# Kernel tuning notes

Hardware: AMD Instinct MI355X
Metric: run time of the kernel (lower is better)

The kernel has to match this reference:

```python
import jax, jax.numpy as jnp
import numpy as np

USER_NUM = 100000
ITEM_NUM = 50000
N_EDGES = 2000000
EMB = 64
N_LAYERS = 3


def setup_inputs() -> dict:
    key = jax.random.key(0)
    k1, k2, k3, k4 = jax.random.split(key, 4)
    # xavier-uniform-like init scale for embeddings
    scale = float(np.sqrt(6.0 / (USER_NUM + EMB)))
    user_emb = jax.random.uniform(k1, (USER_NUM, EMB), jnp.float32, -scale, scale)
    scale_i = float(np.sqrt(6.0 / (ITEM_NUM + EMB)))
    item_emb = jax.random.uniform(k2, (ITEM_NUM, EMB), jnp.float32, -scale_i, scale_i)
    u_idx = jax.random.randint(k3, (N_EDGES,), 0, USER_NUM, jnp.int32)
    i_idx = jax.random.randint(k4, (N_EDGES,), 0, ITEM_NUM, jnp.int32)
    return {"user_emb": user_emb, "item_emb": item_emb, "u_idx": u_idx, "i_idx": i_idx}


def _degree_norms(u_idx, i_idx):
    ones = jnp.ones(u_idx.shape[0], jnp.float32)
    d_u = jax.ops.segment_sum(ones, u_idx, num_segments=USER_NUM)
    d_i = jax.ops.segment_sum(ones, i_idx, num_segments=ITEM_NUM)
    d_u = jnp.where(d_u == 0, 1.0, d_u)
    d_i = jnp.where(d_i == 0, 1.0, d_i)
    return ((1.0 / d_u)[:, None], (1.0 / d_i)[:, None],
            (d_u ** -0.5)[:, None], (d_i ** -0.5)[:, None])


def reference(user_emb, item_emb, u_idx, i_idx):
    d_u_inv, d_i_inv, d_u_inv_sqrt, d_i_inv_sqrt = _degree_norms(u_idx, i_idx)

    # SpMM via gather + segment_sum on the edge list (binary interaction values)
    def spmm_rt(x_u):  # (rt @ x_u): [U,D] -> [I,D]
        return jax.ops.segment_sum(x_u[u_idx], i_idx, num_segments=ITEM_NUM)

    def spmm_r(x_i):  # (r @ x_i): [I,D] -> [U,D]
        return jax.ops.segment_sum(x_i[i_idx], u_idx, num_segments=USER_NUM)

    user_e = user_emb
    item_e = item_emb
    sum_u = user_e
    sum_i = item_e
    for _ in range(N_LAYERS):
        # user propagation: u -> hyperedge(items) -> u
        tmp_u = user_e * d_u_inv_sqrt
        tmp_i = spmm_rt(tmp_u) * d_i_inv
        user_e = spmm_r(tmp_i) * d_u_inv_sqrt
        sum_u = sum_u + user_e
        # item propagation: i -> hyperedge(users) -> i
        tmp_i2 = item_e * d_i_inv_sqrt
        tmp_u2 = spmm_r(tmp_i2) * d_u_inv
        item_e = spmm_rt(tmp_u2) * d_i_inv_sqrt
        sum_i = sum_i + item_e
    inv = 1.0 / (N_LAYERS + 1)
    return sum_u * inv, sum_i * inv
```

## Files before the change

kernel.cpp:

```cpp
#include <hip/hip_runtime.h>
#include <hip/hip_fp16.h>
#include <math.h>

#define U_NUM 100000
#define I_NUM 50000
#define NE    2000000
#define EMB   64
#define NLAYERS 3

#define BSH   9
#define BROWS 512
#define NBU_U ((U_NUM + 511) >> 9)
#define NBU_I ((I_NUM + 511) >> 9)
#define NBU_T (NBU_U + NBU_I)
#define CHUNK 8192
#define NBLK_E ((NE + CHUNK - 1) / CHUNK)
#define DBINS 512
#define PACK_SH 17
#define PACK_MASK 0x1FFFF

#define FP8_SCALE 512.0f

typedef float v2f __attribute__((ext_vector_type(2)));

static inline int ceil_div(int a, int b){ return (a + b - 1) / b; }


__global__ void hist_k(const int* __restrict__ u_idx, const int* __restrict__ i_idx,
                       int* __restrict__ cm_u, int* __restrict__ cm_i,
                       int* __restrict__ dhist_u, int* __restrict__ dhist_i){
  if (blockIdx.x == 0){
    for (int t = threadIdx.x; t < DBINS; t += 256) dhist_u[t] = 0;
  } else if (blockIdx.x == 1){
    for (int t = threadIdx.x; t < DBINS; t += 256) dhist_i[t] = 0;
  }
  __shared__ int h[NBU_T];
  for (int t = threadIdx.x; t < NBU_T; t += 256) h[t] = 0;
  __syncthreads();
  int base = blockIdx.x * CHUNK;
  int end = min(base + CHUNK, NE);
  for (int e = base + (threadIdx.x << 1); e < end; e += 512){
    int2 uu = *(const int2*)(u_idx + e);
    int2 ii = *(const int2*)(i_idx + e);
    atomicAdd(&h[uu.x >> BSH], 1);
    atomicAdd(&h[uu.y >> BSH], 1);
    atomicAdd(&h[NBU_U + (ii.x >> BSH)], 1);
    atomicAdd(&h[NBU_U + (ii.y >> BSH)], 1);
  }
  __syncthreads();
  for (int t = threadIdx.x; t < NBU_U; t += 256) cm_u[blockIdx.x * NBU_U + t] = h[t];
  for (int t = threadIdx.x; t < NBU_I; t += 256) cm_i[blockIdx.x * NBU_I + t] = h[NBU_U + t];
}

__global__ void colsum_k(const int* __restrict__ cm_u, const int* __restrict__ cm_i,
                         int* __restrict__ tot_u, int* __restrict__ tot_i){
  __shared__ int s[256];
  int j = blockIdx.x;
  const int* cm; int* tot; int jj, stride;
  if (j < NBU_U){ cm = cm_u; tot = tot_u; jj = j; stride = NBU_U; }
  else { cm = cm_i; tot = tot_i; jj = j - NBU_U; stride = NBU_I; }
  int acc = 0;
  for (int b = threadIdx.x; b < NBLK_E; b += 256) acc += cm[b * stride + jj];
  s[threadIdx.x] = acc; __syncthreads();
  for (int o = 128; o > 0; o >>= 1){
    if (threadIdx.x < o) s[threadIdx.x] += s[threadIdx.x + o];
    __syncthreads();
  }
  if (threadIdx.x == 0) tot[jj] = s[0];
}

__global__ void small_scan2_k(const int* __restrict__ cA, int* __restrict__ oA,
                              int* __restrict__ rA, int nA,
                              const int* __restrict__ cB, int* __restrict__ oB,
                              int* __restrict__ rB, int nB){
  const int* cnt; int* offs; int* cur; int n;
  if (blockIdx.x == 0){ cnt = cA; offs = oA; cur = rA; n = nA; }
  else { cnt = cB; offs = oB; cur = rB; n = nB; }
  __shared__ int s[1024];
  int t = threadIdx.x;
  int v = (t < n) ? cnt[t] : 0;
  s[t] = v; __syncthreads();
  for (int o = 1; o < 1024; o <<= 1){
    int x = (t >= o) ? s[t - o] : 0;
    __syncthreads();
    s[t] += x;
    __syncthreads();
  }
  int excl = (t > 0) ? s[t - 1] : 0;
  if (t < n){ offs[t] = excl; cur[t] = excl; }
  if (t == n - 1) offs[n] = s[t];
}

__global__ void colscan_k(const int* __restrict__ cm_u, const int* __restrict__ cm_i,
                          const int* __restrict__ boffs_u, const int* __restrict__ boffs_i,
                          int* __restrict__ bm_u, int* __restrict__ bm_i){
  __shared__ int s[256];
  int j = blockIdx.x;
  const int* cm; const int* boffs; int* bm; int jj, stride;
  if (j < NBU_U){ cm = cm_u; boffs = boffs_u; bm = bm_u; jj = j; stride = NBU_U; }
  else { cm = cm_i; boffs = boffs_i; bm = bm_i; jj = j - NBU_U; stride = NBU_I; }
  int t = threadIdx.x;
  int v = (t < NBLK_E) ? cm[t * stride + jj] : 0;
  s[t] = v; __syncthreads();
  for (int o = 1; o < 256; o <<= 1){
    int x = (t >= o) ? s[t - o] : 0;
    __syncthreads();
    s[t] += x;
    __syncthreads();
  }
  int excl = (t > 0) ? s[t - 1] : 0;
  if (t < NBLK_E) bm[t * stride + jj] = excl + boffs[jj];
}


__global__ void binfill_k(const int* __restrict__ u_idx, const int* __restrict__ i_idx,
                          const int* __restrict__ bm_u, const int* __restrict__ bm_i,
                          int* __restrict__ bin_u, int* __restrict__ bin_i){
  __shared__ int cur[NBU_T];
  for (int t = threadIdx.x; t < NBU_U; t += 256) cur[t] = bm_u[blockIdx.x * NBU_U + t];
  for (int t = threadIdx.x; t < NBU_I; t += 256) cur[NBU_U + t] = bm_i[blockIdx.x * NBU_I + t];
  __syncthreads();
  int base = blockIdx.x * CHUNK;
  int end = min(base + CHUNK, NE);
  for (int e = base + (threadIdx.x << 1); e < end; e += 512){
    int2 uu = *(const int2*)(u_idx + e);
    int2 ii = *(const int2*)(i_idx + e);
    int p;
    p = atomicAdd(&cur[uu.x >> BSH], 1);            bin_u[p] = ((uu.x & 511) << PACK_SH) | ii.x;
    p = atomicAdd(&cur[uu.y >> BSH], 1);            bin_u[p] = ((uu.y & 511) << PACK_SH) | ii.y;
    p = atomicAdd(&cur[NBU_U + (ii.x >> BSH)], 1);  bin_i[p] = ((ii.x & 511) << PACK_SH) | uu.x;
    p = atomicAdd(&cur[NBU_U + (ii.y >> BSH)], 1);  bin_i[p] = ((ii.y & 511) << PACK_SH) | uu.y;
  }
}


__global__ void bucket_build_k(const int* __restrict__ bin_u, const int* __restrict__ bin_i,
                               const int* __restrict__ boffs_u, const int* __restrict__ boffs_i,
                               int* __restrict__ cnt_u, int* __restrict__ cnt_i,
                               int* __restrict__ offs_u, int* __restrict__ offs_i,
                               float* __restrict__ du_inv, float* __restrict__ du_invs,
                               float* __restrict__ di_inv, float* __restrict__ di_invs,
                               int* __restrict__ adj_u, int* __restrict__ adj_i,
                               int* __restrict__ dhist_u, int* __restrict__ dhist_i){
  __shared__ int h[BROWS];
  __shared__ int part[256];
  __shared__ int dh[DBINS];
  int b = blockIdx.x;
  const int* bin; const int* boffs; int* cnt; int* offs; float* inv; float* invs;
  int* adj; int* dhist; int jj, nrows;
  if (b < NBU_U){
    bin = bin_u; boffs = boffs_u; cnt = cnt_u; offs = offs_u;
    inv = du_inv; invs = du_invs; adj = adj_u; dhist = dhist_u; jj = b; nrows = U_NUM;
  } else {
    bin = bin_i; boffs = boffs_i; cnt = cnt_i; offs = offs_i;
    inv = di_inv; invs = di_invs; adj = adj_i; dhist = dhist_i; jj = b - NBU_U; nrows = I_NUM;
  }
  int tid = threadIdx.x;
  int r0 = jj << BSH;
  int beg = boffs[jj], end = boffs[jj + 1];
  h[2*tid] = 0; h[2*tid + 1] = 0;
  for (int t = tid; t < DBINS; t += 256) dh[t] = 0;
  __syncthreads();
  for (int e = beg + tid; e < end; e += 256)
    atomicAdd(&h[((unsigned)bin[e]) >> PACK_SH], 1);
  __syncthreads();
  int c0 = h[2*tid], c1 = h[2*tid + 1];
  part[tid] = c0 + c1; __syncthreads();
  for (int o = 1; o < 256; o <<= 1){
    int x = (tid >= o) ? part[tid - o] : 0;
    __syncthreads();
    part[tid] += x;
    __syncthreads();
  }
  int excl = (tid > 0) ? part[tid - 1] : 0;
  h[2*tid] = excl;
  h[2*tid + 1] = excl + c0;
#pragma unroll
  for (int k = 0; k < 2; ++k){
    int l = 2*tid + k;
    int row = r0 + l;
    int c = k ? c1 : c0;
    int o = k ? (excl + c0) : excl;
    if (row < nrows){
      cnt[row] = c;
      offs[row] = beg + o;
      float d = (c > 0) ? (float)c : 1.0f;
      inv[row]  = 1.0f / d;
      invs[row] = 1.0f / sqrtf(d);
      atomicAdd(&dh[min(c, DBINS - 1)], 1);
    } else if (row == nrows){
      offs[row] = beg + o;
    }
  }
  __syncthreads();
  for (int e = beg + tid; e < end; e += 256){
    int v = bin[e];
    int slot = beg + atomicAdd(&h[((unsigned)v) >> PACK_SH], 1);
    adj[slot] = v & PACK_MASK;
  }
  __syncthreads();
  for (int t = tid; t < DBINS; t += 256) if (dh[t]) atomicAdd(&dhist[t], dh[t]);
}


__global__ void deg_scatter_k(const int* __restrict__ cnt, const int* __restrict__ offs,
                              int* __restrict__ dcur, int4* __restrict__ rd, int n){
  __shared__ int h[DBINS];
  __shared__ int base_s[DBINS];
  for (int t = threadIdx.x; t < DBINS; t += 256) h[t] = 0;
  __syncthreads();
  int base = blockIdx.x * 2048;
  int end = min(base + 2048, n);
  for (int r = base + threadIdx.x; r < end; r += 256)
    atomicAdd(&h[min(cnt[r], DBINS - 1)], 1);
  __syncthreads();
  for (int t = threadIdx.x; t < DBINS; t += 256){
    int c = h[t];
    base_s[t] = c ? atomicAdd(&dcur[t], c) : 0;
    h[t] = 0;
  }
  __syncthreads();
  for (int r = base + threadIdx.x; r < end; r += 256){
    int c = cnt[r];
    int b = min(c, DBINS - 1);
    int pos = base_s[b] + atomicAdd(&h[b], 1);
    int bg = offs[r];
    rd[n - 1 - pos] = make_int4(bg, bg + c, r, 0);
  }
}


__device__ __forceinline__ unsigned pack4_fp8(float a, float b, float c, float d){
  int p = 0;
  p = __builtin_amdgcn_cvt_pk_fp8_f32(a, b, p, false);
  p = __builtin_amdgcn_cvt_pk_fp8_f32(c, d, p, true);
  return (unsigned)p;
}

__device__ __forceinline__ void accq(float* a, uint2 q){
  v2f f0 = __builtin_amdgcn_cvt_pk_f32_fp8(q.x, false);
  v2f f1 = __builtin_amdgcn_cvt_pk_f32_fp8(q.x, true);
  v2f f2 = __builtin_amdgcn_cvt_pk_f32_fp8(q.y, false);
  v2f f3 = __builtin_amdgcn_cvt_pk_f32_fp8(q.y, true);
  a[0] += f0.x; a[1] += f0.y; a[2] += f1.x; a[3] += f1.y;
  a[4] += f2.x; a[5] += f2.y; a[6] += f3.x; a[7] += f3.y;
}


__global__ void init_k(const float* __restrict__ ue, const float* __restrict__ ie,
                       const float* __restrict__ dus, const float* __restrict__ dis,
                       float* __restrict__ out, unsigned char* __restrict__ ue8,
                       unsigned char* __restrict__ ie8){
  int idx4 = blockIdx.x * blockDim.x + threadIdx.x;
  const int nu4 = U_NUM * (EMB / 4);
  const int tot4 = (U_NUM + I_NUM) * (EMB / 4);
  if (idx4 >= tot4) return;
  const float* e; unsigned char* hp; float s; int loc;
  if (idx4 < nu4){ e = ue; hp = ue8; loc = idx4; s = dus[idx4 >> 4] * FP8_SCALE; }
  else { e = ie; hp = ie8; loc = idx4 - nu4; s = dis[(idx4 - nu4) >> 4] * FP8_SCALE; }
  float4 v = ((const float4*)e)[loc];
  float4 o = make_float4(v.x * 0.25f, v.y * 0.25f, v.z * 0.25f, v.w * 0.25f);
  ((float4*)out)[idx4] = o;
  ((unsigned*)hp)[loc] = pack4_fp8(v.x * s, v.y * s, v.z * s, v.w * s);
}


template<bool HAS_SUM>
__global__ void spmm_pair(
    const int4* __restrict__ rdA, const int* __restrict__ adjA,
    const unsigned char* __restrict__ srcA, const float* __restrict__ psA, const float* __restrict__ phA,
    unsigned char* __restrict__ dstA, float* __restrict__ sumA, int nA,
    const int4* __restrict__ rdB, const int* __restrict__ adjB,
    const unsigned char* __restrict__ srcB, const float* __restrict__ psB, const float* __restrict__ phB,
    unsigned char* __restrict__ dstB, float* __restrict__ sumB, int nB){
  int t = blockIdx.x * blockDim.x + threadIdx.x;
  int rid = t >> 3;
  int lane = t & 7;
  const int4* rd; const int* adj; const unsigned char* src; const float* ps; const float* ph;
  unsigned char* dst; float* sum;
  if (rid < nA){
    rd = rdA; adj = adjA; src = srcA; ps = psA; ph = phA; dst = dstA; sum = sumA;
  } else {
    rid -= nA;
    if (rid >= nB) return;
    rd = rdB; adj = adjB; src = srcB; ps = psB; ph = phB; dst = dstB; sum = sumB;
  }
  int4 d = rd[rid];
  int beg = d.x, end = d.y, row = d.z;
  const unsigned char* sp8 = src + (size_t)(lane << 3);
  float acc[8];
#pragma unroll
  for (int k = 0; k < 8; ++k) acc[k] = 0.f;
  int j = beg;
  for (; j + 7 < end; j += 8){
    int n0 = adj[j],   n1 = adj[j+1], n2 = adj[j+2], n3 = adj[j+3];
    int n4 = adj[j+4], n5 = adj[j+5], n6 = adj[j+6], n7 = adj[j+7];
    uint2 q0 = *(const uint2*)(sp8 + (((size_t)n0) << 6));
    uint2 q1 = *(const uint2*)(sp8 + (((size_t)n1) << 6));
    uint2 q2 = *(const uint2*)(sp8 + (((size_t)n2) << 6));
    uint2 q3 = *(const uint2*)(sp8 + (((size_t)n3) << 6));
    uint2 q4 = *(const uint2*)(sp8 + (((size_t)n4) << 6));
    uint2 q5 = *(const uint2*)(sp8 + (((size_t)n5) << 6));
    uint2 q6 = *(const uint2*)(sp8 + (((size_t)n6) << 6));
    uint2 q7 = *(const uint2*)(sp8 + (((size_t)n7) << 6));
    accq(acc, q0); accq(acc, q1); accq(acc, q2); accq(acc, q3);
    accq(acc, q4); accq(acc, q5); accq(acc, q6); accq(acc, q7);
  }
  for (; j < end; ++j){
    int n0 = adj[j];
    uint2 q0 = *(const uint2*)(sp8 + (((size_t)n0) << 6));
    accq(acc, q0);
  }
  float phv = ph[row];
  unsigned lo = pack4_fp8(acc[0] * phv, acc[1] * phv, acc[2] * phv, acc[3] * phv);
  unsigned hi = pack4_fp8(acc[4] * phv, acc[5] * phv, acc[6] * phv, acc[7] * phv);
  *(uint2*)(dst + (((size_t)row) << 6) + (size_t)(lane << 3)) = make_uint2(lo, hi);
  if (HAS_SUM){
    float psv = ps[row] * (0.25f / FP8_SCALE);
    float4* sp = (float4*)(sum + (((size_t)row) << 6) + (size_t)(lane << 3));
#pragma unroll
    for (int k = 0; k < 2; ++k){
      float4 s = sp[k];
      s.x += acc[4*k]     * psv;
      s.y += acc[4*k + 1] * psv;
      s.z += acc[4*k + 2] * psv;
      s.w += acc[4*k + 3] * psv;
      sp[k] = s;
    }
  }
}


extern "C" void kernel_launch(void* const* d_in, const int* in_sizes, int n_in,
                              void* d_out, int out_size, void* d_ws, size_t ws_size,
                              hipStream_t stream){
  const float* user_emb = (const float*)d_in[0];
  const float* item_emb = (const float*)d_in[1];
  const int*   u_idx    = (const int*)d_in[2];
  const int*   i_idx    = (const int*)d_in[3];
  float* out = (float*)d_out;

  char* w = (char*)d_ws;
  size_t off = 0;
  auto alloc = [&](size_t bytes) -> void* {
    void* p = (void*)(w + off);
    off += (bytes + 255) & ~(size_t)255;
    return p;
  };
  int* cnt_u   = (int*)alloc((size_t)U_NUM * 4);
  int* cnt_i   = (int*)alloc((size_t)I_NUM * 4);
  int* offs_u  = (int*)alloc((size_t)(U_NUM + 1) * 4);
  int* offs_i  = (int*)alloc((size_t)(I_NUM + 1) * 4);
  int* cm_u    = (int*)alloc((size_t)NBLK_E * NBU_U * 4);
  int* cm_i    = (int*)alloc((size_t)NBLK_E * NBU_I * 4);
  int* bm_u    = (int*)alloc((size_t)NBLK_E * NBU_U * 4);
  int* bm_i    = (int*)alloc((size_t)NBLK_E * NBU_I * 4);
  int* tot_u   = (int*)alloc((size_t)NBU_U * 4);
  int* tot_i   = (int*)alloc((size_t)NBU_I * 4);
  int* boffs_u = (int*)alloc((size_t)(NBU_U + 1) * 4);
  int* boffs_i = (int*)alloc((size_t)(NBU_I + 1) * 4);
  int* scr_u   = (int*)alloc((size_t)NBU_U * 4);
  int* scr_i   = (int*)alloc((size_t)NBU_I * 4);
  int* dhist_u = (int*)alloc((size_t)DBINS * 4);
  int* dhist_i = (int*)alloc((size_t)DBINS * 4);
  int* doffs_u = (int*)alloc((size_t)(DBINS + 1) * 4);
  int* doffs_i = (int*)alloc((size_t)(DBINS + 1) * 4);
  int* dcur_u  = (int*)alloc((size_t)DBINS * 4);
  int* dcur_i  = (int*)alloc((size_t)DBINS * 4);
  int4* rd_u   = (int4*)alloc((size_t)U_NUM * 16);
  int4* rd_i   = (int4*)alloc((size_t)I_NUM * 16);
  int* adj_u   = (int*)alloc((size_t)NE * 4);
  int* adj_i   = (int*)alloc((size_t)NE * 4);
  float* du_inv  = (float*)alloc((size_t)U_NUM * 4);
  float* du_invs = (float*)alloc((size_t)U_NUM * 4);
  float* di_inv  = (float*)alloc((size_t)I_NUM * 4);
  float* di_invs = (float*)alloc((size_t)I_NUM * 4);
  unsigned char* hreg = (unsigned char*)alloc((size_t)(U_NUM + I_NUM) * 128);
  unsigned char* ue8    = hreg;
  unsigned char* ie8    = ue8    + (size_t)U_NUM * EMB;
  unsigned char* tmp_i8 = ie8    + (size_t)I_NUM * EMB;
  unsigned char* tmp_u8 = tmp_i8 + (size_t)I_NUM * EMB;
  int* bin_u = (int*)hreg;
  int* bin_i = bin_u + NE;

  hist_k<<<NBLK_E, 256, 0, stream>>>(u_idx, i_idx, cm_u, cm_i, dhist_u, dhist_i);
  colsum_k<<<NBU_T, 256, 0, stream>>>(cm_u, cm_i, tot_u, tot_i);
  small_scan2_k<<<2, 1024, 0, stream>>>(tot_u, boffs_u, scr_u, NBU_U,
                                        tot_i, boffs_i, scr_i, NBU_I);
  colscan_k<<<NBU_T, 256, 0, stream>>>(cm_u, cm_i, boffs_u, boffs_i, bm_u, bm_i);
  binfill_k<<<NBLK_E, 256, 0, stream>>>(u_idx, i_idx, bm_u, bm_i, bin_u, bin_i);
  bucket_build_k<<<NBU_T, 256, 0, stream>>>(bin_u, bin_i, boffs_u, boffs_i,
                                            cnt_u, cnt_i, offs_u, offs_i,
                                            du_inv, du_invs, di_inv, di_invs,
                                            adj_u, adj_i, dhist_u, dhist_i);

  small_scan2_k<<<2, 1024, 0, stream>>>(dhist_u, doffs_u, dcur_u, DBINS,
                                        dhist_i, doffs_i, dcur_i, DBINS);
  deg_scatter_k<<<ceil_div(U_NUM, 2048), 256, 0, stream>>>(cnt_u, offs_u, dcur_u, rd_u, U_NUM);
  deg_scatter_k<<<ceil_div(I_NUM, 2048), 256, 0, stream>>>(cnt_i, offs_i, dcur_i, rd_i, I_NUM);

  init_k<<<ceil_div((U_NUM + I_NUM) * EMB / 4, 256), 256, 0, stream>>>(
      user_emb, item_emb, du_invs, di_invs, out, ue8, ie8);

  float* sum_u = out;
  float* sum_i = out + (size_t)U_NUM * EMB;
  const int pair_grid = ceil_div((U_NUM + I_NUM) * 8, 256);
  for (int l = 0; l < NLAYERS; ++l){
    spmm_pair<false><<<pair_grid, 256, 0, stream>>>(
        rd_i, adj_i, ue8, nullptr, di_inv, tmp_i8, nullptr, I_NUM,
        rd_u, adj_u, ie8, nullptr, du_inv, tmp_u8, nullptr, U_NUM);
    spmm_pair<true><<<pair_grid, 256, 0, stream>>>(
        rd_u, adj_u, tmp_i8, du_invs, du_inv, ue8, sum_u, U_NUM,
        rd_i, adj_i, tmp_u8, di_invs, di_inv, ie8, sum_i, I_NUM);
  }
}
```

Before: 515.4 us.

## Defer layer-sum accumulation to final merge and fuse setup kernels

Removes the per-layer fp32 read-modify-write of the output sum from the SpMM kernel. Each layer's fp8 result now goes to its own buffer, and one merge kernel accumulates all three into the output at the end, recovering the scale from the ratio of invs to inv. Two small scan kernels are folded into colscan and a new post kernel, which also absorbs deg_scatter and init, cutting launch count. The cost is extra fp8 buffers, one extra pass over the embeddings, and a redundant per-block prefix scan of the degree histogram.

```diff
diff --git a/kernel.cpp b/kernel.cpp
--- a/kernel.cpp
+++ b/kernel.cpp
@@ -19,6 +19,10 @@
 #define PACK_SH 17
 #define PACK_MASK 0x1FFFF
 
+#define ND_U ((U_NUM + 2047) / 2048)
+#define ND_I ((I_NUM + 2047) / 2048)
+#define NINIT (((U_NUM + I_NUM) * (EMB / 4) + 255) / 256)
+
 #define FP8_SCALE 512.0f
 
 typedef float v2f __attribute__((ext_vector_type(2)));
@@ -28,11 +32,16 @@
 
 __global__ void hist_k(const int* __restrict__ u_idx, const int* __restrict__ i_idx,
                        int* __restrict__ cm_u, int* __restrict__ cm_i,
-                       int* __restrict__ dhist_u, int* __restrict__ dhist_i){
+                       int* __restrict__ dhist_u, int* __restrict__ dhist_i,
+                       int* __restrict__ dcur_u, int* __restrict__ dcur_i){
   if (blockIdx.x == 0){
     for (int t = threadIdx.x; t < DBINS; t += 256) dhist_u[t] = 0;
   } else if (blockIdx.x == 1){
     for (int t = threadIdx.x; t < DBINS; t += 256) dhist_i[t] = 0;
+  } else if (blockIdx.x == 2){
+    for (int t = threadIdx.x; t < DBINS; t += 256) dcur_u[t] = 0;
+  } else if (blockIdx.x == 3){
+    for (int t = threadIdx.x; t < DBINS; t += 256) dcur_i[t] = 0;
   }
   __shared__ int h[NBU_T];
   for (int t = threadIdx.x; t < NBU_T; t += 256) h[t] = 0;
@@ -69,37 +78,30 @@
   if (threadIdx.x == 0) tot[jj] = s[0];
 }
 
-__global__ void small_scan2_k(const int* __restrict__ cA, int* __restrict__ oA,
-                              int* __restrict__ rA, int nA,
-                              const int* __restrict__ cB, int* __restrict__ oB,
-                              int* __restrict__ rB, int nB){
-  const int* cnt; int* offs; int* cur; int n;
-  if (blockIdx.x == 0){ cnt = cA; offs = oA; cur = rA; n = nA; }
-  else { cnt = cB; offs = oB; cur = rB; n = nB; }
-  __shared__ int s[1024];
-  int t = threadIdx.x;
-  int v = (t < n) ? cnt[t] : 0;
-  s[t] = v; __syncthreads();
-  for (int o = 1; o < 1024; o <<= 1){
-    int x = (t >= o) ? s[t - o] : 0;
-    __syncthreads();
-    s[t] += x;
-    __syncthreads();
-  }
-  int excl = (t > 0) ? s[t - 1] : 0;
-  if (t < n){ offs[t] = excl; cur[t] = excl; }
-  if (t == n - 1) offs[n] = s[t];
-}
-
 __global__ void colscan_k(const int* __restrict__ cm_u, const int* __restrict__ cm_i,
-                          const int* __restrict__ boffs_u, const int* __restrict__ boffs_i,
+                          const int* __restrict__ tot_u, const int* __restrict__ tot_i,
+                          int* __restrict__ boffs_u, int* __restrict__ boffs_i,
                           int* __restrict__ bm_u, int* __restrict__ bm_i){
   __shared__ int s[256];
+  __shared__ int red[256];
+  __shared__ int bj;
   int j = blockIdx.x;
-  const int* cm; const int* boffs; int* bm; int jj, stride;
-  if (j < NBU_U){ cm = cm_u; boffs = boffs_u; bm = bm_u; jj = j; stride = NBU_U; }
-  else { cm = cm_i; boffs = boffs_i; bm = bm_i; jj = j - NBU_U; stride = NBU_I; }
+  const int* cm; const int* tot; int* boffs; int* bm; int jj, stride, nbu;
+  if (j < NBU_U){ cm = cm_u; tot = tot_u; boffs = boffs_u; bm = bm_u; jj = j; stride = NBU_U; nbu = NBU_U; }
+  else { cm = cm_i; tot = tot_i; boffs = boffs_i; bm = bm_i; jj = j - NBU_U; stride = NBU_I; nbu = NBU_I; }
   int t = threadIdx.x;
+  int my = 0;
+  for (int k = t; k < jj; k += 256) my += tot[k];
+  red[t] = my; __syncthreads();
+  for (int o = 128; o > 0; o >>= 1){
+    if (t < o) red[t] += red[t + o];
+    __syncthreads();
+  }
+  if (t == 0){
+    bj = red[0];
+    boffs[jj] = red[0];
+    if (jj == nbu - 1) boffs[nbu] = red[0] + tot[jj];
+  }
   int v = (t < NBLK_E) ? cm[t * stride + jj] : 0;
   s[t] = v; __syncthreads();
   for (int o = 1; o < 256; o <<= 1){
@@ -109,7 +111,7 @@
     __syncthreads();
   }
   int excl = (t > 0) ? s[t - 1] : 0;
-  if (t < NBLK_E) bm[t * stride + jj] = excl + boffs[jj];
+  if (t < NBLK_E) bm[t * stride + jj] = excl + bj;
 }
 
 
@@ -203,33 +205,6 @@
 }
 
 
-__global__ void deg_scatter_k(const int* __restrict__ cnt, const int* __restrict__ offs,
-                              int* __restrict__ dcur, int4* __restrict__ rd, int n){
-  __shared__ int h[DBINS];
-  __shared__ int base_s[DBINS];
-  for (int t = threadIdx.x; t < DBINS; t += 256) h[t] = 0;
-  __syncthreads();
-  int base = blockIdx.x * 2048;
-  int end = min(base + 2048, n);
-  for (int r = base + threadIdx.x; r < end; r += 256)
-    atomicAdd(&h[min(cnt[r], DBINS - 1)], 1);
-  __syncthreads();
-  for (int t = threadIdx.x; t < DBINS; t += 256){
-    int c = h[t];
-    base_s[t] = c ? atomicAdd(&dcur[t], c) : 0;
-    h[t] = 0;
-  }
-  __syncthreads();
-  for (int r = base + threadIdx.x; r < end; r += 256){
-    int c = cnt[r];
-    int b = min(c, DBINS - 1);
-    int pos = base_s[b] + atomicAdd(&h[b], 1);
-    int bg = offs[r];
-    rd[n - 1 - pos] = make_int4(bg, bg + c, r, 0);
-  }
-}
-
-
 __device__ __forceinline__ unsigned pack4_fp8(float a, float b, float c, float d){
   int p = 0;
   p = __builtin_amdgcn_cvt_pk_fp8_f32(a, b, p, false);
@@ -247,43 +222,86 @@
 }
 
 
-__global__ void init_k(const float* __restrict__ ue, const float* __restrict__ ie,
+__global__ void post_k(const int* __restrict__ cnt_u, const int* __restrict__ offs_u,
+                       const int* __restrict__ dhist_u, int* __restrict__ dcur_u,
+                       int4* __restrict__ rd_u,
+                       const int* __restrict__ cnt_i, const int* __restrict__ offs_i,
+                       const int* __restrict__ dhist_i, int* __restrict__ dcur_i,
+                       int4* __restrict__ rd_i,
+                       const float* __restrict__ ue, const float* __restrict__ ie,
                        const float* __restrict__ dus, const float* __restrict__ dis,
-                       float* __restrict__ out, unsigned char* __restrict__ ue8,
-                       unsigned char* __restrict__ ie8){
-  int idx4 = blockIdx.x * blockDim.x + threadIdx.x;
-  const int nu4 = U_NUM * (EMB / 4);
-  const int tot4 = (U_NUM + I_NUM) * (EMB / 4);
-  if (idx4 >= tot4) return;
-  const float* e; unsigned char* hp; float s; int loc;
-  if (idx4 < nu4){ e = ue; hp = ue8; loc = idx4; s = dus[idx4 >> 4] * FP8_SCALE; }
-  else { e = ie; hp = ie8; loc = idx4 - nu4; s = dis[(idx4 - nu4) >> 4] * FP8_SCALE; }
-  float4 v = ((const float4*)e)[loc];
-  float4 o = make_float4(v.x * 0.25f, v.y * 0.25f, v.z * 0.25f, v.w * 0.25f);
-  ((float4*)out)[idx4] = o;
-  ((unsigned*)hp)[loc] = pack4_fp8(v.x * s, v.y * s, v.z * s, v.w * s);
-}
-
-
-template<bool HAS_SUM>
+                       float* __restrict__ out, unsigned char* __restrict__ u0,
+                       unsigned char* __restrict__ i0){
+  int b = blockIdx.x;
+  int t = threadIdx.x;
+  if (b >= ND_U + ND_I){
+    int idx4 = (b - ND_U - ND_I) * 256 + t;
+    const int nu4 = U_NUM * (EMB / 4);
+    const int tot4 = (U_NUM + I_NUM) * (EMB / 4);
+    if (idx4 >= tot4) return;
+    const float* e; unsigned char* hp; float s; int loc;
+    if (idx4 < nu4){ e = ue; hp = u0; loc = idx4; s = dus[idx4 >> 4] * FP8_SCALE; }
+    else { e = ie; hp = i0; loc = idx4 - nu4; s = dis[(idx4 - nu4) >> 4] * FP8_SCALE; }
+    float4 v = ((const float4*)e)[loc];
+    ((float4*)out)[idx4] = make_float4(v.x * 0.25f, v.y * 0.25f, v.z * 0.25f, v.w * 0.25f);
+    ((unsigned*)hp)[loc] = pack4_fp8(v.x * s, v.y * s, v.z * s, v.w * s);
+    return;
+  }
+  const int* cnt; const int* offs; const int* dhist; int* dcur; int4* rd; int n, base;
+  if (b < ND_U){ cnt = cnt_u; offs = offs_u; dhist = dhist_u; dcur = dcur_u; rd = rd_u; n = U_NUM; base = b * 2048; }
+  else { cnt = cnt_i; offs = offs_i; dhist = dhist_i; dcur = dcur_i; rd = rd_i; n = I_NUM; base = (b - ND_U) * 2048; }
+  __shared__ int sc[DBINS];
+  __shared__ int h[DBINS];
+  __shared__ int base_s[DBINS];
+  sc[t] = dhist[t]; sc[t + 256] = dhist[t + 256];
+  h[t] = 0; h[t + 256] = 0;
+  __syncthreads();
+  for (int o = 1; o < DBINS; o <<= 1){
+    int x0 = (t >= o) ? sc[t - o] : 0;
+    int x1 = ((t + 256) >= o) ? sc[t + 256 - o] : 0;
+    __syncthreads();
+    sc[t] += x0; sc[t + 256] += x1;
+    __syncthreads();
+  }
+  int end = min(base + 2048, n);
+  for (int r = base + t; r < end; r += 256)
+    atomicAdd(&h[min(cnt[r], DBINS - 1)], 1);
+  __syncthreads();
+  for (int tt = t; tt < DBINS; tt += 256){
+    int c = h[tt];
+    int excl = tt ? sc[tt - 1] : 0;
+    base_s[tt] = c ? (excl + atomicAdd(&dcur[tt], c)) : 0;
+    h[tt] = 0;
+  }
+  __syncthreads();
+  for (int r = base + t; r < end; r += 256){
+    int c = cnt[r];
+    int bb = min(c, DBINS - 1);
+    int pos = base_s[bb] + atomicAdd(&h[bb], 1);
+    int bg = offs[r];
+    rd[n - 1 - pos] = make_int4(bg, bg + c, r, 0);
+  }
+}
+
+
 __global__ void spmm_pair(
     const int4* __restrict__ rdA, const int* __restrict__ adjA,
-    const unsigned char* __restrict__ srcA, const float* __restrict__ psA, const float* __restrict__ phA,
-    unsigned char* __restrict__ dstA, float* __restrict__ sumA, int nA,
+    const unsigned char* __restrict__ srcA, const float* __restrict__ phA,
+    unsigned char* __restrict__ dstA, int nA,
     const int4* __restrict__ rdB, const int* __restrict__ adjB,
-    const unsigned char* __restrict__ srcB, const float* __restrict__ psB, const float* __restrict__ phB,
-    unsigned char* __restrict__ dstB, float* __restrict__ sumB, int nB){
+    const unsigned char* __restrict__ srcB, const float* __restrict__ phB,
+    unsigned char* __restrict__ dstB, int nB){
   int t = blockIdx.x * blockDim.x + threadIdx.x;
   int rid = t >> 3;
   int lane = t & 7;
-  const int4* rd; const int* adj; const unsigned char* src; const float* ps; const float* ph;
-  unsigned char* dst; float* sum;
+  const int4* rd; const int* adj; const unsigned char* src; const float* ph;
+  unsigned char* dst;
   if (rid < nA){
-    rd = rdA; adj = adjA; src = srcA; ps = psA; ph = phA; dst = dstA; sum = sumA;
+    rd = rdA; adj = adjA; src = srcA; ph = phA; dst = dstA;
   } else {
     rid -= nA;
     if (rid >= nB) return;
-    rd = rdB; adj = adjB; src = srcB; ps = psB; ph = phB; dst = dstB; sum = sumB;
+    rd = rdB; adj = adjB; src = srcB; ph = phB; dst = dstB;
   }
   int4 d = rd[rid];
   int beg = d.x, end = d.y, row = d.z;
@@ -315,19 +333,43 @@
   unsigned lo = pack4_fp8(acc[0] * phv, acc[1] * phv, acc[2] * phv, acc[3] * phv);
   unsigned hi = pack4_fp8(acc[4] * phv, acc[5] * phv, acc[6] * phv, acc[7] * phv);
   *(uint2*)(dst + (((size_t)row) << 6) + (size_t)(lane << 3)) = make_uint2(lo, hi);
-  if (HAS_SUM){
-    float psv = ps[row] * (0.25f / FP8_SCALE);
-    float4* sp = (float4*)(sum + (((size_t)row) << 6) + (size_t)(lane << 3));
-#pragma unroll
-    for (int k = 0; k < 2; ++k){
-      float4 s = sp[k];
-      s.x += acc[4*k]     * psv;
-      s.y += acc[4*k + 1] * psv;
-      s.z += acc[4*k + 2] * psv;
-      s.w += acc[4*k + 3] * psv;
-      sp[k] = s;
-    }
-  }
+}
+
+
+__global__ void merge_k(const unsigned char* __restrict__ u1, const unsigned char* __restrict__ u2,
+                        const unsigned char* __restrict__ u3,
+                        const unsigned char* __restrict__ i1, const unsigned char* __restrict__ i2,
+                        const unsigned char* __restrict__ i3,
+                        const float* __restrict__ du_inv, const float* __restrict__ du_invs,
+                        const float* __restrict__ di_inv, const float* __restrict__ di_invs,
+                        float* __restrict__ out){
+  int idx4 = blockIdx.x * blockDim.x + threadIdx.x;
+  const int nu4 = U_NUM * (EMB / 4);
+  const int tot4 = (U_NUM + I_NUM) * (EMB / 4);
+  if (idx4 >= tot4) return;
+  const unsigned char *t1, *t2, *t3; float ratio; int loc;
+  if (idx4 < nu4){
+    t1 = u1; t2 = u2; t3 = u3; loc = idx4;
+    int row = idx4 >> 4;
+    ratio = (0.25f / FP8_SCALE) * du_invs[row] / du_inv[row];
+  } else {
+    loc = idx4 - nu4;
+    t1 = i1; t2 = i2; t3 = i3;
+    int row = loc >> 4;
+    ratio = (0.25f / FP8_SCALE) * di_invs[row] / di_inv[row];
+  }
+  unsigned q1 = ((const unsigned*)t1)[loc];
+  unsigned q2 = ((const unsigned*)t2)[loc];
+  unsigned q3 = ((const unsigned*)t3)[loc];
+  float4 o = ((float4*)out)[idx4];
+  v2f a, b;
+  a = __builtin_amdgcn_cvt_pk_f32_fp8(q1, false); b = __builtin_amdgcn_cvt_pk_f32_fp8(q1, true);
+  o.x += ratio * a.x; o.y += ratio * a.y; o.z += ratio * b.x; o.w += ratio * b.y;
+  a = __builtin_amdgcn_cvt_pk_f32_fp8(q2, false); b = __builtin_amdgcn_cvt_pk_f32_fp8(q2, true);
+  o.x += ratio * a.x; o.y += ratio * a.y; o.z += ratio * b.x; o.w += ratio * b.y;
+  a = __builtin_amdgcn_cvt_pk_f32_fp8(q3, false); b = __builtin_amdgcn_cvt_pk_f32_fp8(q3, true);
+  o.x += ratio * a.x; o.y += ratio * a.y; o.z += ratio * b.x; o.w += ratio * b.y;
+  ((float4*)out)[idx4] = o;
 }
 
 
@@ -359,12 +401,8 @@
   int* tot_i   = (int*)alloc((size_t)NBU_I * 4);
   int* boffs_u = (int*)alloc((size_t)(NBU_U + 1) * 4);
   int* boffs_i = (int*)alloc((size_t)(NBU_I + 1) * 4);
-  int* scr_u   = (int*)alloc((size_t)NBU_U * 4);
-  int* scr_i   = (int*)alloc((size_t)NBU_I * 4);
   int* dhist_u = (int*)alloc((size_t)DBINS * 4);
   int* dhist_i = (int*)alloc((size_t)DBINS * 4);
-  int* doffs_u = (int*)alloc((size_t)(DBINS + 1) * 4);
-  int* doffs_i = (int*)alloc((size_t)(DBINS + 1) * 4);
   int* dcur_u  = (int*)alloc((size_t)DBINS * 4);
   int* dcur_i  = (int*)alloc((size_t)DBINS * 4);
   int4* rd_u   = (int4*)alloc((size_t)U_NUM * 16);
@@ -375,42 +413,49 @@
   float* du_invs = (float*)alloc((size_t)U_NUM * 4);
   float* di_inv  = (float*)alloc((size_t)I_NUM * 4);
   float* di_invs = (float*)alloc((size_t)I_NUM * 4);
-  unsigned char* hreg = (unsigned char*)alloc((size_t)(U_NUM + I_NUM) * 128);
-  unsigned char* ue8    = hreg;
-  unsigned char* ie8    = ue8    + (size_t)U_NUM * EMB;
-  unsigned char* tmp_i8 = ie8    + (size_t)I_NUM * EMB;
-  unsigned char* tmp_u8 = tmp_i8 + (size_t)I_NUM * EMB;
+  const size_t URB = (size_t)U_NUM * EMB;
+  const size_t IRB = (size_t)I_NUM * EMB;
+  unsigned char* hreg = (unsigned char*)alloc(4 * URB + 4 * IRB + URB + IRB);
+  unsigned char* u0 = hreg;
+  unsigned char* u1 = u0 + URB;
+  unsigned char* u2 = u1 + URB;
+  unsigned char* u3 = u2 + URB;
+  unsigned char* i0 = u3 + URB;
+  unsigned char* i1 = i0 + IRB;
+  unsigned char* i2 = i1 + IRB;
+  unsigned char* i3 = i2 + IRB;
+  unsigned char* tmp_i = i3 + IRB;
+  unsigned char* tmp_u = tmp_i + IRB;
   int* bin_u = (int*)hreg;
   int* bin_i = bin_u + NE;
 
-  hist_k<<<NBLK_E, 256, 0, stream>>>(u_idx, i_idx, cm_u, cm_i, dhist_u, dhist_i);
+  hist_k<<<NBLK_E, 256, 0, stream>>>(u_idx, i_idx, cm_u, cm_i, dhist_u, dhist_i, dcur_u, dcur_i);
   colsum_k<<<NBU_T, 256, 0, stream>>>(cm_u, cm_i, tot_u, tot_i);
-  small_scan2_k<<<2, 1024, 0, stream>>>(tot_u, boffs_u, scr_u, NBU_U,
-                                        tot_i, boffs_i, scr_i, NBU_I);
-  colscan_k<<<NBU_T, 256, 0, stream>>>(cm_u, cm_i, boffs_u, boffs_i, bm_u, bm_i);
+  colscan_k<<<NBU_T, 256, 0, stream>>>(cm_u, cm_i, tot_u, tot_i,
+                                       boffs_u, boffs_i, bm_u, bm_i);
   binfill_k<<<NBLK_E, 256, 0, stream>>>(u_idx, i_idx, bm_u, bm_i, bin_u, bin_i);
   bucket_build_k<<<NBU_T, 256, 0, stream>>>(bin_u, bin_i, boffs_u, boffs_i,
                                             cnt_u, cnt_i, offs_u, offs_i,
                                             du_inv, du_invs, di_inv, di_invs,
                                             adj_u, adj_i, dhist_u, dhist_i);
 
-  small_scan2_k<<<2, 1024, 0, stream>>>(dhist_u, doffs_u, dcur_u, DBINS,
-                                        dhist_i, doffs_i, dcur_i, DBINS);
-  deg_scatter_k<<<ceil_div(U_NUM, 2048), 256, 0, stream>>>(cnt_u, offs_u, dcur_u, rd_u, U_NUM);
-  deg_scatter_k<<<ceil_div(I_NUM, 2048), 256, 0, stream>>>(cnt_i, offs_i, dcur_i, rd_i, I_NUM);
-
-  init_k<<<ceil_div((U_NUM + I_NUM) * EMB / 4, 256), 256, 0, stream>>>(
-      user_emb, item_emb, du_invs, di_invs, out, ue8, ie8);
-
-  float* sum_u = out;
-  float* sum_i = out + (size_t)U_NUM * EMB;
+  post_k<<<ND_U + ND_I + NINIT, 256, 0, stream>>>(
+      cnt_u, offs_u, dhist_u, dcur_u, rd_u,
+      cnt_i, offs_i, dhist_i, dcur_i, rd_i,
+      user_emb, item_emb, du_invs, di_invs, out, u0, i0);
+
   const int pair_grid = ceil_div((U_NUM + I_NUM) * 8, 256);
+  unsigned char* uls[4] = { u0, u1, u2, u3 };
+  unsigned char* ils[4] = { i0, i1, i2, i3 };
   for (int l = 0; l < NLAYERS; ++l){
-    spmm_pair<false><<<pair_grid, 256, 0, stream>>>(
-        rd_i, adj_i, ue8, nullptr, di_inv, tmp_i8, nullptr, I_NUM,
-        rd_u, adj_u, ie8, nullptr, du_inv, tmp_u8, nullptr, U_NUM);
-    spmm_pair<true><<<pair_grid, 256, 0, stream>>>(
-        rd_u, adj_u, tmp_i8, du_invs, du_inv, ue8, sum_u, U_NUM,
-        rd_i, adj_i, tmp_u8, di_invs, di_inv, ie8, sum_i, I_NUM);
-  }
-}
+    spmm_pair<<<pair_grid, 256, 0, stream>>>(
+        rd_i, adj_i, uls[l], di_inv, tmp_i, I_NUM,
+        rd_u, adj_u, ils[l], du_inv, tmp_u, U_NUM);
+    spmm_pair<<<pair_grid, 256, 0, stream>>>(
+        rd_u, adj_u, tmp_i, du_inv, uls[l + 1], U_NUM,
+        rd_i, adj_i, tmp_u, di_inv, ils[l + 1], I_NUM);
+  }
+
+  merge_k<<<NINIT, 256, 0, stream>>>(u1, u2, u3, i1, i2, i3,
+                                     du_inv, du_invs, di_inv, di_invs, out);
+}
```

Measured after the change: 489.7 us. 5.0% less time.
